# Performance work log

Hardware: AMD Instinct MI355X
Metric: run time of the kernel (lower is better)

Reference implementation:

```python
import jax, jax.numpy as jnp
import numpy as np

RADIUS = 0.1
NSAMPLE = 32
EPS = 1e-5


def ball_query(radius, nsample, xyz):
    # xyz: [B, N, 3] -> idx [B, N, nsample] (query set == support set)
    B, N, _ = xyz.shape
    # pairwise squared distances [B, N, N]
    sq = jnp.sum((xyz[:, :, None, :] - xyz[:, None, :, :]) ** 2, axis=-1)
    grp = jnp.broadcast_to(jnp.arange(N, dtype=jnp.int32), (B, N, N))
    grp = jnp.where(sq > radius * radius, N, grp)
    grp = jnp.sort(grp, axis=-1)[:, :, :nsample]
    first = grp[:, :, 0:1]
    return jnp.where(grp == N, first, grp)  # self is always in-ball -> first valid


def index_points(points, idx):
    # points [B, N, C], idx [B, N, S] -> [B, N, S, C]
    B, N, S = idx.shape
    C = points.shape[-1]
    flat = jnp.take_along_axis(points, idx.reshape(B, N * S, 1), axis=1)
    return flat.reshape(B, N, S, C)


def bn(x, gamma, beta, mean, var, axis):
    # eval-mode batchnorm over channel axis
    shape = [1] * x.ndim
    shape[axis] = -1
    g = gamma.reshape(shape); b = beta.reshape(shape)
    m = mean.reshape(shape); v = var.reshape(shape)
    return (x - m) * (g * jax.lax.rsqrt(v + EPS)) + b


def setup_inputs() -> dict:
    key = jax.random.key(0)
    ks = jax.random.split(key, 8)
    B, N, C, E = 4, 4096, 128, 4
    H = C * E
    xyz = jax.random.uniform(ks[0], (B, N, 3), dtype=jnp.float32)
    feats = jax.random.normal(ks[1], (B, N, C), dtype=jnp.float32)
    s = 0.05
    Wn = jax.random.normal(ks[2], (C, C + 3), dtype=jnp.float32) * s
    W1 = jax.random.normal(ks[3], (H, C), dtype=jnp.float32) * s
    W2 = jax.random.normal(ks[4], (C, H), dtype=jnp.float32) * s
    def bnp(k, n):
        k1, k2 = jax.random.split(k)
        return (jnp.ones((n,), jnp.float32) + 0.01 * jax.random.normal(k1, (n,)),
                0.01 * jax.random.normal(k2, (n,)),
                jnp.zeros((n,), jnp.float32),
                jnp.ones((n,), jnp.float32))
    gn, bn_, mn, vn = bnp(ks[5], C)
    g1, b1, m1, v1 = bnp(ks[6], H)
    g2, b2, m2, v2 = bnp(ks[7], C)
    return dict(xyz=xyz, feats=feats, Wn=Wn, gn=gn, bn_=bn_, mn=mn, vn=vn,
                W1=W1, g1=g1, b1=b1, m1=m1, v1=v1,
                W2=W2, g2=g2, b2=b2, m2=m2, v2=v2)


def reference(xyz, feats, Wn, gn, bn_, mn, vn, W1, g1, b1, m1, v1, W2, g2, b2, m2, v2):
    B, N, C = feats.shape
    identity = feats  # [B, N, C]
    idx = ball_query(RADIUS, NSAMPLE, xyz)  # [B, N, S]
    grouped_xyz = index_points(xyz, idx) - xyz[:, :, None, :]  # [B, N, S, 3]
    grouped_xyz = grouped_xyz / RADIUS  # normalize_dp
    grouped_feats = index_points(feats, idx)  # [B, N, S, C]
    grouped = jnp.concatenate([grouped_xyz, grouped_feats], axis=-1)  # [B, N, S, C+3]
    # torch layout [B, C+3, S, N]; keep [B, N, S, C+3] and contract channels
    x = jnp.einsum('oc,bnsc->bnso', Wn, grouped)  # neighbor 1x1 conv
    x = jax.nn.relu(bn(x, gn, bn_, mn, vn, axis=3))
    x = jnp.max(x, axis=2)  # max over neighbors -> [B, N, C]
    # inverted bottleneck pointwise MLP
    h = jnp.einsum('hc,bnc->bnh', W1, x)
    h = jax.nn.relu(bn(h, g1, b1, m1, v1, axis=2))
    y = jnp.einsum('ch,bnh->bnc', W2, h)
    y = bn(y, g2, b2, m2, v2, axis=2)
    out = jax.nn.relu(y + identity)  # [B, N, C]
    return out
```

## Files before the change

### kernel.cpp

```cpp
#include <hip/hip_runtime.h>
#include <hip/hip_bf16.h>
#include <math.h>

static constexpr int BB = 4;
static constexpr int NN = 4096;
static constexpr int CC = 128;
static constexpr int HH = 512;
static constexpr int SS = 32;
static constexpr float EPSF = 1e-5f;
static constexpr int NCELL = 1000;

typedef __bf16 bf16_t;
typedef bf16_t bf16x8 __attribute__((ext_vector_type(8)));
typedef float f32x4 __attribute__((ext_vector_type(4)));
typedef float f32x2 __attribute__((ext_vector_type(2)));

__device__ inline unsigned short f2bf(float f) {
    unsigned int u = __builtin_bit_cast(unsigned int, f);
    u += 0x7FFFu + ((u >> 16) & 1u);
    return (unsigned short)(u >> 16);
}
__device__ inline float u2f(unsigned int u) {
    return __builtin_bit_cast(float, u);
}
__device__ inline int cell_of(float v) {
    int c = (int)(v * 10.0f);
    return c > 9 ? 9 : (c < 0 ? 0 : c);
}
__device__ inline f32x2 pk_fma_b(f32x2 a, float g, f32x2 c) {
    const f32x2 gg = {g, g};
    return a * gg + c;
}

__device__ inline void gload_lds16(const void* g, void* l) {
    __builtin_amdgcn_global_load_lds(
        (const __attribute__((address_space(1))) unsigned int*)g,
        (__attribute__((address_space(3))) unsigned int*)l, 16, 0, 0);
}

__global__ __launch_bounds__(256)
void prep_kernel(const float* __restrict__ Wn, const float* __restrict__ W1,
                 const float* __restrict__ W2,
                 const float* __restrict__ gn, const float* __restrict__ bnv,
                 const float* __restrict__ mn, const float* __restrict__ vn,
                 unsigned short* __restrict__ WnF, unsigned short* __restrict__ W1b,
                 unsigned short* __restrict__ W2b, float4* __restrict__ wfold)
{
    const int blk = blockIdx.x;
    const int t   = threadIdx.x;
    if (blk < 576) {
        const int i = blk * 256 + t;
        if (i < 16384) {
            const int o = i >> 7, c = i & 127;
            WnF[i] = f2bf(Wn[o * 131 + 3 + c]);
        } else if (i < 16384 + 65536) {
            const int k = i - 16384;
            W1b[k] = f2bf(W1[k]);
        } else if (i < 16384 + 131072) {
            const int k = i - 16384 - 65536;
            W2b[k] = f2bf(W2[k]);
        }
    } else {
        if (t < CC) {
            const float sc = gn[t] / sqrtf(vn[t] + EPSF);
            wfold[t] = make_float4(sc * Wn[t * 131 + 0], sc * Wn[t * 131 + 1],
                                   sc * Wn[t * 131 + 2], bnv[t] - mn[t] * sc);
        }
    }
}

__global__ __launch_bounds__(1024)
void bin_kernel(const float* __restrict__ xyz, int* __restrict__ starts,
                float4* __restrict__ spts)
{
    const int b = blockIdx.x;
    const int t = threadIdx.x;

    __shared__ int cur[1024];
    __shared__ int ls[1024];

    cur[t] = 0;
    __syncthreads();

    int    cid[4];
    float4 pt[4];
    #pragma unroll
    for (int k = 0; k < 4; ++k) {
        const int n = k * 1024 + t;
        const float x = xyz[((size_t)b * NN + n) * 3 + 0];
        const float y = xyz[((size_t)b * NN + n) * 3 + 1];
        const float z = xyz[((size_t)b * NN + n) * 3 + 2];
        cid[k] = cell_of(z) * 100 + cell_of(y) * 10 + cell_of(x);
        pt[k]  = make_float4(x, y, z, __int_as_float(n));
        atomicAdd(&cur[cid[k]], 1);
    }
    __syncthreads();

    const int v = cur[t];
    ls[t] = v;
    __syncthreads();
    #pragma unroll
    for (int off = 1; off < 1024; off <<= 1) {
        const int add = (t >= off) ? ls[t - off] : 0;
        __syncthreads();
        ls[t] += add;
        __syncthreads();
    }
    const int ex = ls[t] - v;
    if (t < NCELL) starts[b * NCELL + t] = b * NN + ex;
    if (b == 0 && t == 0) starts[BB * NCELL] = BB * NN;
    __syncthreads();
    cur[t] = ex;
    __syncthreads();

    #pragma unroll
    for (int k = 0; k < 4; ++k) {
        const int pos = atomicAdd(&cur[cid[k]], 1);
        spts[(size_t)b * NN + pos] = pt[k];
    }
}

__global__ __launch_bounds__(64)
void ball_query_binned_kernel(const float* __restrict__ xyz,
                              const int* __restrict__ starts,
                              const float4* __restrict__ spts,
                              int* __restrict__ idx)
{
    const int p    = blockIdx.x;
    const int b    = p >> 12;
    const int lane = threadIdx.x;

    const float qx = xyz[p * 3 + 0];
    const float qy = xyz[p * 3 + 1];
    const float qz = xyz[p * 3 + 2];
    const int cx = cell_of(qx), cy = cell_of(qy), cz = cell_of(qz);
    const int xlo = cx > 0 ? cx - 1 : 0;
    const int xhi = cx < 9 ? cx + 1 : 9;

    __shared__ int list[128];
    __shared__ int res[SS];
    int cnt = 0;

    for (int dz = -1; dz <= 1; ++dz) {
        const int z2 = cz + dz;
        if (z2 < 0 || z2 > 9) continue;
        for (int dy = -1; dy <= 1; ++dy) {
            const int y2 = cy + dy;
            if (y2 < 0 || y2 > 9) continue;
            const int base = b * NCELL + z2 * 100 + y2 * 10;
            const int lo = starts[base + xlo];
            const int hi = starts[base + xhi + 1];
            for (int j0 = lo; j0 < hi; j0 += 64) {
                const int j = j0 + lane;
                bool in = false;
                int pi = 0;
                if (j < hi) {
                    const float4 s = spts[j];
                    float sq;
                    {
                        #pragma clang fp contract(off)
                        const float dx  = qx - s.x;
                        const float dyv = qy - s.y;
                        const float dzv = qz - s.z;
                        sq = dx * dx + dyv * dyv + dzv * dzv;
                    }
                    in = (sq <= 0.01f);
                    pi = __float_as_int(s.w);
                }
                const unsigned long long mask = __ballot(in);
                if (in) {
                    const int pos = cnt + __popcll(mask & ((1ull << lane) - 1ull));
                    if (pos < 128) list[pos] = pi;
                }
                cnt += (int)__popcll(mask);
            }
        }
    }
    __syncthreads();

    const int c = cnt < 128 ? cnt : 128;
    #pragma unroll
    for (int l0 = 0; l0 < 2; ++l0) {
        const int l = lane + l0 * 64;
        if (l < c) {
            const int v = list[l];
            int r = 0;
            for (int k = 0; k < c; ++k) r += (list[k] < v);
            if (r < SS) res[r] = v;
        }
    }
    __syncthreads();

    if (lane < SS) {
        const int m = c < SS ? c : SS;
        idx[(size_t)p * SS + lane] = (lane < m) ? res[lane] : res[0];
    }
}

__global__ __launch_bounds__(256)
void group_max_kernel(const float* __restrict__ xyz,
                      const unsigned short* __restrict__ T,
                      const float4* __restrict__ wfold,
                      const int* __restrict__ idx, unsigned short* __restrict__ xout)
{
    const int t   = threadIdx.x;
    const int ptl = t >> 5;
    const int l   = t & 31;
    const int p   = blockIdx.x * 8 + ptl;
    const int b   = p >> 12;

    __shared__ float4 sg[8][32];

    {
        const int j = idx[(size_t)p * SS + l];
        const float* q  = xyz + (size_t)p * 3;
        const float* pj = xyz + ((size_t)b * NN + j) * 3;
        sg[ptl][l] = make_float4((pj[0] - q[0]) / 0.1f,
                                 (pj[1] - q[1]) / 0.1f,
                                 (pj[2] - q[2]) / 0.1f, __int_as_float(j));
    }
    __syncthreads();

    const int c0 = l * 4;
    const float4 wa = wfold[c0 + 0], wb = wfold[c0 + 1];
    const float4 wc = wfold[c0 + 2], wd = wfold[c0 + 3];
    const f32x2 w0p0 = {wa.x, wb.x}, w1p0 = {wa.y, wb.y}, w2p0 = {wa.z, wb.z};
    const f32x2 w0p1 = {wc.x, wd.x}, w1p1 = {wc.y, wd.y}, w2p1 = {wc.z, wd.z};

    const unsigned short* Tb = T + (size_t)b * NN * CC;
    f32x2 mx0 = {-1e30f, -1e30f}, mx1 = {-1e30f, -1e30f};

    #pragma unroll 8
    for (int s = 0; s < SS; ++s) {
        const float4 g = sg[ptl][s];
        const int j = __float_as_int(g.w);
        const uint2 tv = *(const uint2*)(Tb + (size_t)j * CC + c0);
        f32x2 v0, v1;
        v0.x = u2f(tv.x << 16); v0.y = u2f(tv.x & 0xFFFF0000u);
        v1.x = u2f(tv.y << 16); v1.y = u2f(tv.y & 0xFFFF0000u);
        v0 = pk_fma_b(w0p0, g.x, v0); v0 = pk_fma_b(w1p0, g.y, v0); v0 = pk_fma_b(w2p0, g.z, v0);
        v1 = pk_fma_b(w0p1, g.x, v1); v1 = pk_fma_b(w1p1, g.y, v1); v1 = pk_fma_b(w2p1, g.z, v1);
        mx0.x = fmaxf(mx0.x, v0.x); mx0.y = fmaxf(mx0.y, v0.y);
        mx1.x = fmaxf(mx1.x, v1.x); mx1.y = fmaxf(mx1.y, v1.y);
    }

    const float r0 = fmaxf(mx0.x + wa.w, 0.f);
    const float r1 = fmaxf(mx0.y + wb.w, 0.f);
    const float r2 = fmaxf(mx1.x + wc.w, 0.f);
    const float r3 = fmaxf(mx1.y + wd.w, 0.f);
    uint2 o;
    o.x = (unsigned)f2bf(r0) | ((unsigned)f2bf(r1) << 16);
    o.y = (unsigned)f2bf(r2) | ((unsigned)f2bf(r3) << 16);
    *(uint2*)(xout + (size_t)p * CC + c0) = o;
}

template<int MODE, int BNt>
__global__ __launch_bounds__(256, 2)
void mfma_gemm_kernel(const unsigned short* __restrict__ A, const unsigned short* __restrict__ W,
                      const float* __restrict__ g, const float* __restrict__ bb,
                      const float* __restrict__ mu, const float* __restrict__ var,
                      const float* __restrict__ res, void* __restrict__ outv,
                      int M, int Nout, int K)
{
    constexpr int BM = 64, BK = 64;
    constexpr int NF = BNt / 32;
    __shared__ char smem[(BM + BNt) * BK * 2];
    char* sA = smem;
    char* sB = smem + BM * BK * 2;

    const int t    = threadIdx.x;
    const int lane = t & 63;
    const int w    = t >> 6;
    const int wm   = w >> 1;
    const int wn   = w & 1;
    const int m0   = blockIdx.x * BM;
    const int o0   = blockIdx.y * BNt;
    const int Kb   = K * 2;

    f32x4 acc[2][NF];
    #pragma unroll
    for (int i = 0; i < 2; ++i)
        #pragma unroll
        for (int j = 0; j < NF; ++j) acc[i][j] = f32x4{0.f, 0.f, 0.f, 0.f};

    const char* Ab = (const char*)A;
    const float* Af = (const float*)A;
    const char* Wb = (const char*)W;

    for (int kc = 0; kc < K; kc += BK) {
        const int kcb = kc * 2;
        #pragma unroll
        for (int l = 0; l < 2; ++l) {
            const int q     = w * 2 + l;
            const int Lb    = q * 1024 + lane * 16;
            const int row   = Lb >> 7;
            const int inrow = Lb & 127;
            const int sw    = inrow ^ ((row & 7) << 4);
            if constexpr (MODE == 3) {
                const float* src = Af + (size_t)(m0 + row) * K + kc + (sw >> 1);
                const float4 a0 = *(const float4*)(src);
                const float4 a1 = *(const float4*)(src + 4);
                uint4 pk;
                pk.x = (unsigned)f2bf(a0.x) | ((unsigned)f2bf(a0.y) << 16);
                pk.y = (unsigned)f2bf(a0.z) | ((unsigned)f2bf(a0.w) << 16);
                pk.z = (unsigned)f2bf(a1.x) | ((unsigned)f2bf(a1.y) << 16);
                pk.w = (unsigned)f2bf(a1.z) | ((unsigned)f2bf(a1.w) << 16);
                *(uint4*)(sA + Lb) = pk;
            } else {
                const char* src = Ab + (size_t)(m0 + row) * Kb + kcb + sw;
                gload_lds16(src, sA + q * 1024);
            }
        }
        #pragma unroll
        for (int l = 0; l < NF; ++l) {
            const int q     = w * NF + l;
            const int Lb    = q * 1024 + lane * 16;
            const int row   = Lb >> 7;
            const int inrow = Lb & 127;
            const char* src = Wb + (size_t)(o0 + row) * Kb + kcb + (inrow ^ ((row & 7) << 4));
            gload_lds16(src, sB + q * 1024);
        }
        __syncthreads();

        #pragma unroll
        for (int ks = 0; ks < 2; ++ks) {
            const int kbyte = ks * 64 + (lane >> 4) * 16;
            bf16x8 af[2], bf[NF];
            #pragma unroll
            for (int i = 0; i < 2; ++i) {
                const int r = wm * 32 + i * 16 + (lane & 15);
                af[i] = *(const bf16x8*)(sA + r * 128 + (kbyte ^ ((r & 7) << 4)));
            }
            #pragma unroll
            for (int j = 0; j < NF; ++j) {
                const int r = wn * (BNt / 2) + j * 16 + (lane & 15);
                bf[j] = *(const bf16x8*)(sB + r * 128 + (kbyte ^ ((r & 7) << 4)));
            }
            #pragma unroll
            for (int i = 0; i < 2; ++i)
                #pragma unroll
                for (int j = 0; j < NF; ++j)
                    acc[i][j] = __builtin_amdgcn_mfma_f32_16x16x32_bf16(af[i], bf[j], acc[i][j], 0, 0, 0);
        }
        __syncthreads();
    }

    #pragma unroll
    for (int j = 0; j < NF; ++j) {
        const int col = o0 + wn * (BNt / 2) + j * 16 + (lane & 15);
        float scg = 1.f, sh = 0.f, mm = 0.f;
        if constexpr (MODE == 1 || MODE == 2) {
            scg = g[col] / sqrtf(var[col] + EPSF);
            mm  = mu[col];
            sh  = bb[col];
        }
        if constexpr (MODE == 3) {
            scg = g[col] / sqrtf(var[col] + EPSF);
        }
        #pragma unroll
        for (int i = 0; i < 2; ++i) {
            const int rowb = m0 + wm * 32 + i * 16 + (lane >> 4) * 4;
            #pragma unroll
            for (int r = 0; r < 4; ++r) {
                float z = acc[i][j][r];
                if constexpr (MODE == 1 || MODE == 2) z = (z - mm) * scg + sh;
                if constexpr (MODE == 3) z = z * scg;
                if constexpr (MODE == 2) z += res[(size_t)(rowb + r) * Nout + col];
                if constexpr (MODE == 1 || MODE == 2) z = fmaxf(z, 0.f);
                if constexpr (MODE == 2)
                    ((float*)outv)[(size_t)(rowb + r) * Nout + col] = z;
                else
                    ((unsigned short*)outv)[(size_t)(rowb + r) * Nout + col] = f2bf(z);
            }
        }
    }
}

extern "C" void kernel_launch(void* const* d_in, const int* in_sizes, int n_in,
                              void* d_out, int out_size, void* d_ws, size_t ws_size,
                              hipStream_t stream)
{
    const float* xyz   = (const float*)d_in[0];
    const float* feats = (const float*)d_in[1];
    const float* Wn    = (const float*)d_in[2];
    const float* gn    = (const float*)d_in[3];
    const float* bn_   = (const float*)d_in[4];
    const float* mn    = (const float*)d_in[5];
    const float* vn    = (const float*)d_in[6];
    const float* W1    = (const float*)d_in[7];
    const float* g1    = (const float*)d_in[8];
    const float* b1    = (const float*)d_in[9];
    const float* m1    = (const float*)d_in[10];
    const float* v1    = (const float*)d_in[11];
    const float* W2    = (const float*)d_in[12];
    const float* g2    = (const float*)d_in[13];
    const float* b2    = (const float*)d_in[14];
    const float* m2    = (const float*)d_in[15];
    const float* v2    = (const float*)d_in[16];
    float* out = (float*)d_out;

    char* ws = (char*)d_ws;
    int*            idx    = (int*)(ws);
    int*            starts = (int*)(ws + 2097152);
    float4*         spts   = (float4*)(ws + 2113536);
    unsigned short* WnF    = (unsigned short*)(ws + 2375680);
    unsigned short* W1b    = (unsigned short*)(ws + 2408448);
    unsigned short* W2b    = (unsigned short*)(ws + 2539520);
    unsigned short* Tb     = (unsigned short*)(ws + 2670592);
    unsigned short* xb     = (unsigned short*)(ws + 6864896);
    unsigned short* hb     = (unsigned short*)(ws + 11059200);
    float4*         wfold  = (float4*)(ws + 27836416);

    const int M = BB * NN;

    prep_kernel<<<577, 256, 0, stream>>>(Wn, W1, W2, gn, bn_, mn, vn,
                                         WnF, W1b, W2b, wfold);
    bin_kernel<<<BB, 1024, 0, stream>>>(xyz, starts, spts);
    ball_query_binned_kernel<<<M, 64, 0, stream>>>(xyz, starts, spts, idx);

    mfma_gemm_kernel<3, 128><<<dim3(M / 64, 1), 256, 0, stream>>>(
        (const unsigned short*)feats, WnF, gn, nullptr, nullptr, vn, nullptr, Tb, M, CC, CC);

    group_max_kernel<<<M / 8, 256, 0, stream>>>(xyz, Tb, wfold, idx, xb);

    mfma_gemm_kernel<1, 128><<<dim3(M / 64, HH / 128), 256, 0, stream>>>(
        xb, W1b, g1, b1, m1, v1, nullptr, hb, M, HH, CC);

    mfma_gemm_kernel<2, 64><<<dim3(M / 64, CC / 64), 256, 0, stream>>>(
        hb, W2b, g2, b2, m2, v2, feats, out, M, CC, HH);
}
```

Baseline: 155.9 us.

## Merge prep with binning, and the feature GEMM with ball query, into single launches

Weight conversion and spatial binning now run in one launch, with different block ranges taking different jobs. The first feature-transform GEMM and the ball query are also combined into one kernel, with the first 256 blocks doing the GEMM and the rest doing queries. Each query block now handles four points, one wave per point, instead of one point per 64-thread block. The aim is to cut launch overhead and let the independent GEMM and ball-query work overlap on the GPU, at the cost of a larger shared buffer and 256-thread blocks for the query path.

```diff
diff --git a/kernel.cpp b/kernel.cpp
--- a/kernel.cpp
+++ b/kernel.cpp
@@ -38,47 +38,44 @@
         (__attribute__((address_space(3))) unsigned int*)l, 16, 0, 0);
 }
 
-__global__ __launch_bounds__(256)
-void prep_kernel(const float* __restrict__ Wn, const float* __restrict__ W1,
-                 const float* __restrict__ W2,
-                 const float* __restrict__ gn, const float* __restrict__ bnv,
-                 const float* __restrict__ mn, const float* __restrict__ vn,
-                 unsigned short* __restrict__ WnF, unsigned short* __restrict__ W1b,
-                 unsigned short* __restrict__ W2b, float4* __restrict__ wfold)
+__global__ __launch_bounds__(1024)
+void prep_bin_kernel(const float* __restrict__ Wn, const float* __restrict__ W1,
+                     const float* __restrict__ W2,
+                     const float* __restrict__ gn, const float* __restrict__ bnv,
+                     const float* __restrict__ mn, const float* __restrict__ vn,
+                     const float* __restrict__ xyz,
+                     unsigned short* __restrict__ WnF, unsigned short* __restrict__ W1b,
+                     unsigned short* __restrict__ W2b, float4* __restrict__ wfold,
+                     int* __restrict__ starts, float4* __restrict__ spts)
 {
     const int blk = blockIdx.x;
     const int t   = threadIdx.x;
-    if (blk < 576) {
-        const int i = blk * 256 + t;
+
+    __shared__ int cur[1024];
+    __shared__ int ls[1024];
+
+    if (blk < 144) {
+        const int i = blk * 1024 + t;
         if (i < 16384) {
             const int o = i >> 7, c = i & 127;
             WnF[i] = f2bf(Wn[o * 131 + 3 + c]);
-        } else if (i < 16384 + 65536) {
-            const int k = i - 16384;
-            W1b[k] = f2bf(W1[k]);
-        } else if (i < 16384 + 131072) {
-            const int k = i - 16384 - 65536;
-            W2b[k] = f2bf(W2[k]);
-        }
-    } else {
+        } else if (i < 81920) {
+            W1b[i - 16384] = f2bf(W1[i - 16384]);
+        } else {
+            W2b[i - 81920] = f2bf(W2[i - 81920]);
+        }
+        return;
+    }
+    if (blk == 144) {
         if (t < CC) {
             const float sc = gn[t] / sqrtf(vn[t] + EPSF);
             wfold[t] = make_float4(sc * Wn[t * 131 + 0], sc * Wn[t * 131 + 1],
                                    sc * Wn[t * 131 + 2], bnv[t] - mn[t] * sc);
         }
-    }
-}
-
-__global__ __launch_bounds__(1024)
-void bin_kernel(const float* __restrict__ xyz, int* __restrict__ starts,
-                float4* __restrict__ spts)
-{
-    const int b = blockIdx.x;
-    const int t = threadIdx.x;
-
-    __shared__ int cur[1024];
-    __shared__ int ls[1024];
-
+        return;
+    }
+
+    const int b = blk - 145;
     cur[t] = 0;
     __syncthreads();
 
@@ -120,80 +117,170 @@
     }
 }
 
-__global__ __launch_bounds__(64)
-void ball_query_binned_kernel(const float* __restrict__ xyz,
-                              const int* __restrict__ starts,
-                              const float4* __restrict__ spts,
-                              int* __restrict__ idx)
+__global__ __launch_bounds__(256, 2)
+void tgemm_bq_kernel(const float* __restrict__ feats, const unsigned short* __restrict__ WnF,
+                     const float* __restrict__ gn, const float* __restrict__ vn,
+                     unsigned short* __restrict__ Tb,
+                     const float* __restrict__ xyz, const int* __restrict__ starts,
+                     const float4* __restrict__ spts, int* __restrict__ idx)
 {
-    const int p    = blockIdx.x;
-    const int b    = p >> 12;
-    const int lane = threadIdx.x;
-
-    const float qx = xyz[p * 3 + 0];
-    const float qy = xyz[p * 3 + 1];
-    const float qz = xyz[p * 3 + 2];
-    const int cx = cell_of(qx), cy = cell_of(qy), cz = cell_of(qz);
-    const int xlo = cx > 0 ? cx - 1 : 0;
-    const int xhi = cx < 9 ? cx + 1 : 9;
-
-    __shared__ int list[128];
-    __shared__ int res[SS];
-    int cnt = 0;
-
-    for (int dz = -1; dz <= 1; ++dz) {
-        const int z2 = cz + dz;
-        if (z2 < 0 || z2 > 9) continue;
-        for (int dy = -1; dy <= 1; ++dy) {
-            const int y2 = cy + dy;
-            if (y2 < 0 || y2 > 9) continue;
-            const int base = b * NCELL + z2 * 100 + y2 * 10;
-            const int lo = starts[base + xlo];
-            const int hi = starts[base + xhi + 1];
-            for (int j0 = lo; j0 < hi; j0 += 64) {
-                const int j = j0 + lane;
-                bool in = false;
-                int pi = 0;
-                if (j < hi) {
-                    const float4 s = spts[j];
-                    float sq;
-                    {
-                        #pragma clang fp contract(off)
-                        const float dx  = qx - s.x;
-                        const float dyv = qy - s.y;
-                        const float dzv = qz - s.z;
-                        sq = dx * dx + dyv * dyv + dzv * dzv;
+    __shared__ char smem[(64 + 128) * 128];
+
+    if (blockIdx.x < 256) {
+        char* sA = smem;
+        char* sB = smem + 64 * 128;
+        const int t    = threadIdx.x;
+        const int lane = t & 63;
+        const int w    = t >> 6;
+        const int wm   = w >> 1;
+        const int wn   = w & 1;
+        const int m0   = blockIdx.x * 64;
+
+        f32x4 acc[2][4];
+        #pragma unroll
+        for (int i = 0; i < 2; ++i)
+            #pragma unroll
+            for (int j = 0; j < 4; ++j) acc[i][j] = f32x4{0.f, 0.f, 0.f, 0.f};
+
+        const char* Wb = (const char*)WnF;
+
+        for (int kc = 0; kc < CC; kc += 64) {
+            #pragma unroll
+            for (int l = 0; l < 2; ++l) {
+                const int q     = w * 2 + l;
+                const int Lb    = q * 1024 + lane * 16;
+                const int row   = Lb >> 7;
+                const int inrow = Lb & 127;
+                const int sw    = inrow ^ ((row & 7) << 4);
+                const float* src = feats + (size_t)(m0 + row) * CC + kc + (sw >> 1);
+                const float4 a0 = *(const float4*)(src);
+                const float4 a1 = *(const float4*)(src + 4);
+                uint4 pk;
+                pk.x = (unsigned)f2bf(a0.x) | ((unsigned)f2bf(a0.y) << 16);
+                pk.y = (unsigned)f2bf(a0.z) | ((unsigned)f2bf(a0.w) << 16);
+                pk.z = (unsigned)f2bf(a1.x) | ((unsigned)f2bf(a1.y) << 16);
+                pk.w = (unsigned)f2bf(a1.z) | ((unsigned)f2bf(a1.w) << 16);
+                *(uint4*)(sA + Lb) = pk;
+            }
+            #pragma unroll
+            for (int l = 0; l < 4; ++l) {
+                const int q     = w * 4 + l;
+                const int Lb    = q * 1024 + lane * 16;
+                const int row   = Lb >> 7;
+                const int inrow = Lb & 127;
+                const char* src = Wb + (size_t)row * 256 + kc * 2 + (inrow ^ ((row & 7) << 4));
+                gload_lds16(src, sB + q * 1024);
+            }
+            __syncthreads();
+
+            #pragma unroll
+            for (int ks = 0; ks < 2; ++ks) {
+                const int kbyte = ks * 64 + (lane >> 4) * 16;
+                bf16x8 af[2], bf[4];
+                #pragma unroll
+                for (int i = 0; i < 2; ++i) {
+                    const int r = wm * 32 + i * 16 + (lane & 15);
+                    af[i] = *(const bf16x8*)(sA + r * 128 + (kbyte ^ ((r & 7) << 4)));
+                }
+                #pragma unroll
+                for (int j = 0; j < 4; ++j) {
+                    const int r = wn * 64 + j * 16 + (lane & 15);
+                    bf[j] = *(const bf16x8*)(sB + r * 128 + (kbyte ^ ((r & 7) << 4)));
+                }
+                #pragma unroll
+                for (int i = 0; i < 2; ++i)
+                    #pragma unroll
+                    for (int j = 0; j < 4; ++j)
+                        acc[i][j] = __builtin_amdgcn_mfma_f32_16x16x32_bf16(af[i], bf[j], acc[i][j], 0, 0, 0);
+            }
+            __syncthreads();
+        }
+
+        #pragma unroll
+        for (int j = 0; j < 4; ++j) {
+            const int col = wn * 64 + j * 16 + (lane & 15);
+            const float scg = gn[col] / sqrtf(vn[col] + EPSF);
+            #pragma unroll
+            for (int i = 0; i < 2; ++i) {
+                const int rowb = m0 + wm * 32 + i * 16 + (lane >> 4) * 4;
+                #pragma unroll
+                for (int r = 0; r < 4; ++r)
+                    Tb[(size_t)(rowb + r) * CC + col] = f2bf(acc[i][j][r] * scg);
+            }
+        }
+    } else {
+        const int t    = threadIdx.x;
+        const int wv   = t >> 6;
+        const int lane = t & 63;
+        const int p    = (blockIdx.x - 256) * 4 + wv;
+        const int b    = p >> 12;
+
+        int* lbase = (int*)smem + wv * 160;
+        int* list  = lbase;
+        int* res   = lbase + 128;
+
+        const float qx = xyz[p * 3 + 0];
+        const float qy = xyz[p * 3 + 1];
+        const float qz = xyz[p * 3 + 2];
+        const int cx = cell_of(qx), cy = cell_of(qy), cz = cell_of(qz);
+        const int xlo = cx > 0 ? cx - 1 : 0;
+        const int xhi = cx < 9 ? cx + 1 : 9;
+
+        int cnt = 0;
+        for (int dz = -1; dz <= 1; ++dz) {
+            const int z2 = cz + dz;
+            if (z2 < 0 || z2 > 9) continue;
+            for (int dy = -1; dy <= 1; ++dy) {
+                const int y2 = cy + dy;
+                if (y2 < 0 || y2 > 9) continue;
+                const int base = b * NCELL + z2 * 100 + y2 * 10;
+                const int lo = starts[base + xlo];
+                const int hi = starts[base + xhi + 1];
+                for (int j0 = lo; j0 < hi; j0 += 64) {
+                    const int j = j0 + lane;
+                    bool in = false;
+                    int pi = 0;
+                    if (j < hi) {
+                        const float4 s = spts[j];
+                        float sq;
+                        {
+                            #pragma clang fp contract(off)
+                            const float dx  = qx - s.x;
+                            const float dyv = qy - s.y;
+                            const float dzv = qz - s.z;
+                            sq = dx * dx + dyv * dyv + dzv * dzv;
+                        }
+                        in = (sq <= 0.01f);
+                        pi = __float_as_int(s.w);
                     }
-                    in = (sq <= 0.01f);
-                    pi = __float_as_int(s.w);
+                    const unsigned long long mask = __ballot(in);
+                    if (in) {
+                        const int pos = cnt + __popcll(mask & ((1ull << lane) - 1ull));
+                        if (pos < 128) list[pos] = pi;
+                    }
+                    cnt += (int)__popcll(mask);
                 }
-                const unsigned long long mask = __ballot(in);
-                if (in) {
-                    const int pos = cnt + __popcll(mask & ((1ull << lane) - 1ull));
-                    if (pos < 128) list[pos] = pi;
-                }
-                cnt += (int)__popcll(mask);
-            }
-        }
-    }
-    __syncthreads();
-
-    const int c = cnt < 128 ? cnt : 128;
-    #pragma unroll
-    for (int l0 = 0; l0 < 2; ++l0) {
-        const int l = lane + l0 * 64;
-        if (l < c) {
-            const int v = list[l];
-            int r = 0;
-            for (int k = 0; k < c; ++k) r += (list[k] < v);
-            if (r < SS) res[r] = v;
-        }
-    }
-    __syncthreads();
-
-    if (lane < SS) {
-        const int m = c < SS ? c : SS;
-        idx[(size_t)p * SS + lane] = (lane < m) ? res[lane] : res[0];
+            }
+        }
+        __syncthreads();
+
+        const int c = cnt < 128 ? cnt : 128;
+        #pragma unroll
+        for (int l0 = 0; l0 < 2; ++l0) {
+            const int l = lane + l0 * 64;
+            if (l < c) {
+                const int v = list[l];
+                int r = 0;
+                for (int k = 0; k < c; ++k) r += (list[k] < v);
+                if (r < SS) res[r] = v;
+            }
+        }
+        __syncthreads();
+
+        if (lane < SS) {
+            const int m = c < SS ? c : SS;
+            idx[(size_t)p * SS + lane] = (lane < m) ? res[lane] : res[0];
+        }
     }
 }
 
@@ -227,14 +314,14 @@
     const f32x2 w0p0 = {wa.x, wb.x}, w1p0 = {wa.y, wb.y}, w2p0 = {wa.z, wb.z};
     const f32x2 w0p1 = {wc.x, wd.x}, w1p1 = {wc.y, wd.y}, w2p1 = {wc.z, wd.z};
 
-    const unsigned short* Tb = T + (size_t)b * NN * CC;
+    const unsigned short* Tbp = T + (size_t)b * NN * CC;
     f32x2 mx0 = {-1e30f, -1e30f}, mx1 = {-1e30f, -1e30f};
 
     #pragma unroll 8
     for (int s = 0; s < SS; ++s) {
         const float4 g = sg[ptl][s];
         const int j = __float_as_int(g.w);
-        const uint2 tv = *(const uint2*)(Tb + (size_t)j * CC + c0);
+        const uint2 tv = *(const uint2*)(Tbp + (size_t)j * CC + c0);
         f32x2 v0, v1;
         v0.x = u2f(tv.x << 16); v0.y = u2f(tv.x & 0xFFFF0000u);
         v1.x = u2f(tv.y << 16); v1.y = u2f(tv.y & 0xFFFF0000u);
@@ -284,7 +371,6 @@
         for (int j = 0; j < NF; ++j) acc[i][j] = f32x4{0.f, 0.f, 0.f, 0.f};
 
     const char* Ab = (const char*)A;
-    const float* Af = (const float*)A;
     const char* Wb = (const char*)W;
 
     for (int kc = 0; kc < K; kc += BK) {
@@ -295,21 +381,8 @@
             const int Lb    = q * 1024 + lane * 16;
             const int row   = Lb >> 7;
             const int inrow = Lb & 127;
-            const int sw    = inrow ^ ((row & 7) << 4);
-            if constexpr (MODE == 3) {
-                const float* src = Af + (size_t)(m0 + row) * K + kc + (sw >> 1);
-                const float4 a0 = *(const float4*)(src);
-                const float4 a1 = *(const float4*)(src + 4);
-                uint4 pk;
-                pk.x = (unsigned)f2bf(a0.x) | ((unsigned)f2bf(a0.y) << 16);
-                pk.y = (unsigned)f2bf(a0.z) | ((unsigned)f2bf(a0.w) << 16);
-                pk.z = (unsigned)f2bf(a1.x) | ((unsigned)f2bf(a1.y) << 16);
-                pk.w = (unsigned)f2bf(a1.z) | ((unsigned)f2bf(a1.w) << 16);
-                *(uint4*)(sA + Lb) = pk;
-            } else {
-                const char* src = Ab + (size_t)(m0 + row) * Kb + kcb + sw;
-                gload_lds16(src, sA + q * 1024);
-            }
+            const char* src = Ab + (size_t)(m0 + row) * Kb + kcb + (inrow ^ ((row & 7) << 4));
+            gload_lds16(src, sA + q * 1024);
         }
         #pragma unroll
         for (int l = 0; l < NF; ++l) {
@@ -348,25 +421,18 @@
     #pragma unroll
     for (int j = 0; j < NF; ++j) {
         const int col = o0 + wn * (BNt / 2) + j * 16 + (lane & 15);
-        float scg = 1.f, sh = 0.f, mm = 0.f;
-        if constexpr (MODE == 1 || MODE == 2) {
-            scg = g[col] / sqrtf(var[col] + EPSF);
-            mm  = mu[col];
-            sh  = bb[col];
-        }
-        if constexpr (MODE == 3) {
-            scg = g[col] / sqrtf(var[col] + EPSF);
-        }
+        const float scg = g[col] / sqrtf(var[col] + EPSF);
+        const float mm  = mu[col];
+        const float sh  = bb[col];
         #pragma unroll
         for (int i = 0; i < 2; ++i) {
             const int rowb = m0 + wm * 32 + i * 16 + (lane >> 4) * 4;
             #pragma unroll
             for (int r = 0; r < 4; ++r) {
                 float z = acc[i][j][r];
-                if constexpr (MODE == 1 || MODE == 2) z = (z - mm) * scg + sh;
-                if constexpr (MODE == 3) z = z * scg;
+                z = (z - mm) * scg + sh;
                 if constexpr (MODE == 2) z += res[(size_t)(rowb + r) * Nout + col];
-                if constexpr (MODE == 1 || MODE == 2) z = fmaxf(z, 0.f);
+                z = fmaxf(z, 0.f);
                 if constexpr (MODE == 2)
                     ((float*)outv)[(size_t)(rowb + r) * Nout + col] = z;
                 else
@@ -413,13 +479,11 @@
 
     const int M = BB * NN;
 
-    prep_kernel<<<577, 256, 0, stream>>>(Wn, W1, W2, gn, bn_, mn, vn,
-                                         WnF, W1b, W2b, wfold);
-    bin_kernel<<<BB, 1024, 0, stream>>>(xyz, starts, spts);
-    ball_query_binned_kernel<<<M, 64, 0, stream>>>(xyz, starts, spts, idx);
-
-    mfma_gemm_kernel<3, 128><<<dim3(M / 64, 1), 256, 0, stream>>>(
-        (const unsigned short*)feats, WnF, gn, nullptr, nullptr, vn, nullptr, Tb, M, CC, CC);
+    prep_bin_kernel<<<149, 1024, 0, stream>>>(Wn, W1, W2, gn, bn_, mn, vn, xyz,
+                                              WnF, W1b, W2b, wfold, starts, spts);
+
+    tgemm_bq_kernel<<<256 + M / 4, 256, 0, stream>>>(feats, WnF, gn, vn, Tb,
+                                                     xyz, starts, spts, idx);
 
     group_max_kernel<<<M / 8, 256, 0, stream>>>(xyz, Tb, wfold, idx, xb);
 
```

After: 151.0 us. 3.2% less time.
